# Optimization experiments

Measured on AMD Instinct MI355X. Metric: run time of the kernel, lower is better.

## Reference

```python
import jax, jax.numpy as jnp
import numpy as np

N = 100000      # nodes
E = 1600000     # edges
IN = 4          # input_size
H = 128         # hidden_channels
R = 20          # num_robots
OUT = 2         # output_size


def setup_inputs() -> dict:
    key = jax.random.key(0)
    ks = jax.random.split(key, 9)
    x = jax.random.normal(ks[0], (N, IN), dtype=jnp.float32)
    edge_index = jax.random.randint(ks[1], (2, E), 0, N, dtype=jnp.int32)
    batch = jnp.zeros((N,), dtype=jnp.int32)  # single graph
    # GCNConv weights (glorot-ish) and biases
    W1 = jax.random.normal(ks[2], (IN, H), dtype=jnp.float32) / np.sqrt(IN)
    b1 = jnp.zeros((H,), dtype=jnp.float32)
    W2 = jax.random.normal(ks[3], (H, H), dtype=jnp.float32) / np.sqrt(H)
    b2 = jnp.zeros((H,), dtype=jnp.float32)
    Wfc = jax.random.normal(ks[4], (H, OUT * R), dtype=jnp.float32) / np.sqrt(H)
    bfc = jnp.zeros((OUT * R,), dtype=jnp.float32)
    return {"x": x, "edge_index": edge_index, "batch": batch,
            "W1": W1, "b1": b1, "W2": W2, "b2": b2, "Wfc": Wfc, "bfc": bfc}


def gcn_conv(x, W, b, src, dst, n):
    # PyG GCNConv: h = x @ W, symmetric deg^-1/2 norm (self-loops already in src/dst),
    # aggregate messages at dst, then add bias.
    h = x @ W                                                     # [n, H_out]
    deg = jax.ops.segment_sum(jnp.ones(src.shape[0], h.dtype), dst, num_segments=n)
    dinv = jnp.where(deg > 0, jax.lax.rsqrt(deg), 0.0)            # [n]
    norm = dinv[src] * dinv[dst]                                  # [E+n]
    out = jax.ops.segment_sum(h[src] * norm[:, None], dst, num_segments=n)
    return out + b


def reference(x, edge_index, batch, W1, b1, W2, b2, Wfc, bfc):
    n = x.shape[0]
    loops = jnp.arange(n, dtype=edge_index.dtype)
    src = jnp.concatenate([edge_index[0], loops])   # add self-loops (GCNConv default)
    dst = jnp.concatenate([edge_index[1], loops])

    h = jnp.tanh(gcn_conv(x, W1, b1, src, dst, n))
    h = jnp.tanh(gcn_conv(h, W2, b2, src, dst, n))

    # global_mean_pool over batch (single graph)
    num_graphs = 1
    sums = jax.ops.segment_sum(h, batch, num_segments=num_graphs)           # [G, H]
    cnt = jax.ops.segment_sum(jnp.ones((n,), h.dtype), batch, num_segments=num_graphs)
    pooled = sums / jnp.maximum(cnt, 1.0)[:, None]

    vel = (pooled @ Wfc + bfc).reshape(-1, R, OUT)                          # [G, R, 2]

    # in_size = number of nodes with both first two features nonzero
    in_size = jnp.sum((x[:, 0] != 0.0) & (x[:, 1] != 0.0))
    mask = (jnp.arange(R) < in_size)[None, :, None]
    return jnp.where(mask, vel, 0.0)
```

## Files before the change

### kernel.cpp

```cpp
#include <hip/hip_runtime.h>
#include <hip/hip_fp16.h>

#define NN 100000
#define NE 1600000
#define INF 4
#define H 128
#define RR 20
#define OUTF 2
#define NB 782
#define NBP 784
#define EPB 4096
#define NBLK ((NE + EPB - 1) / EPB)
#define ASPLIT 4

typedef unsigned int uint32;
typedef __attribute__((ext_vector_type(8))) short short8;
typedef __attribute__((ext_vector_type(4))) float f32x4;

__device__ inline uint32 pack_f16(float x, float y) {
    return (uint32)__half_as_ushort(__float2half(x)) |
           ((uint32)__half_as_ushort(__float2half(y)) << 16);
}
__device__ inline __half2 bc_h2(uint32 u) {
    union { uint32 u; __half2 h; } c; c.u = u; return c.h;
}

__global__ void k_init_nodes(const float* __restrict__ x, int* __restrict__ in_size) {
    int i = blockIdx.x * 256 + threadIdx.x;
    bool pred = false;
    if (i < NN) {
        float x0 = x[(size_t)i * INF + 0];
        float x1 = x[(size_t)i * INF + 1];
        pred = (x0 != 0.f) && (x1 != 0.f);
    }
    unsigned long long m = __ballot(pred);
    if ((threadIdx.x & 63) == 0) {
        int c = __popcll(m);
        if (c) atomicAdd(in_size, c);
    }
}

__global__ void __launch_bounds__(256) k_hist(const int* __restrict__ dst,
                                              int* __restrict__ histG) {
    __shared__ int h[NB];
    int b = blockIdx.x, t = threadIdx.x;
    for (int i = t; i < NB; i += 256) h[i] = 0;
    __syncthreads();
    int e0 = b * EPB, eend = min(e0 + EPB, NE);
    for (int e = e0 + t; e < eend; e += 256) atomicAdd(&h[dst[e] >> 7], 1);
    __syncthreads();
    for (int i = t; i < NB; i += 256) histG[b * NBP + i] = h[i];
}

__global__ void k_btotoffs(const int* __restrict__ histG, int* __restrict__ offs,
                           int* __restrict__ btot) {
    int bkt = blockIdx.x * 256 + threadIdx.x;
    if (bkt >= NB) return;
    int run = 0;
    for (int j = 0; j < NBLK; ++j) {
        int v = histG[j * NBP + bkt];
        offs[j * NBP + bkt] = run;
        run += v;
    }
    btot[bkt] = run;
}

__global__ void __launch_bounds__(1024) k_bbase(const int* __restrict__ btot,
                                                int* __restrict__ bbase) {
    __shared__ int sm[1024];
    int t = threadIdx.x;
    int v = (t < NB) ? btot[t] : 0;
    sm[t] = v;
    __syncthreads();
    for (int off = 1; off < 1024; off <<= 1) {
        int u = (t >= off) ? sm[t - off] : 0;
        __syncthreads();
        sm[t] += u;
        __syncthreads();
    }
    if (t < NB) bbase[t] = sm[t] - v;
    if (t == 0) bbase[NB] = NE;
}

__global__ void __launch_bounds__(256) k_scat2(const int* __restrict__ src,
                                               const int* __restrict__ dst,
                                               const int* __restrict__ offs,
                                               const int* __restrict__ bbase,
                                               uint32* __restrict__ data) {
    __shared__ int cur[NB];
    int b = blockIdx.x, t = threadIdx.x;
    for (int i = t; i < NB; i += 256) cur[i] = offs[b * NBP + i] + bbase[i];
    __syncthreads();
    int e0 = b * EPB, eend = min(e0 + EPB, NE);
    for (int e = e0 + t; e < eend; e += 256) {
        int s = src[e], d = dst[e];
        int p = atomicAdd(&cur[d >> 7], 1);
        data[p] = ((uint32)s << 7) | (uint32)(d & 127);
    }
}

__global__ void __launch_bounds__(256) k_build(const uint32* __restrict__ data,
                                               const int* __restrict__ bbase,
                                               const float* __restrict__ x,
                                               int* __restrict__ csr_off,
                                               int* __restrict__ csr_cnt,
                                               int* __restrict__ csr_src,
                                               float* __restrict__ dinv,
                                               float4* __restrict__ xd) {
    __shared__ int hist[128], pfx[128], curs[128];
    int bkt = blockIdx.x;
    int t = threadIdx.x;
    int rbeg = bbase[bkt], rend = bbase[bkt + 1];
    if (t < 128) hist[t] = 0;
    __syncthreads();
    for (int j = rbeg + t; j < rend; j += 256)
        atomicAdd(&hist[data[j] & 127], 1);
    __syncthreads();
    if (t < 128) pfx[t] = hist[t];
    __syncthreads();
    for (int off = 1; off < 128; off <<= 1) {
        int u = (t < 128 && t >= off) ? pfx[t - off] : 0;
        __syncthreads();
        if (t < 128) pfx[t] += u;
        __syncthreads();
    }
    int nodeCount = min(128, NN - bkt * 128);
    if (t < nodeCount) {
        int gi = bkt * 128 + t;
        int excl = rbeg + pfx[t] - hist[t];
        csr_off[gi] = excl;
        csr_cnt[gi] = hist[t];
        curs[t] = excl;
        float di = rsqrtf((float)(hist[t] + 1));
        dinv[gi] = di;
        const float4 xv = *(const float4*)(x + (size_t)gi * INF);
        xd[gi] = make_float4(xv.x * di, xv.y * di, xv.z * di, xv.w * di);
    }
    __syncthreads();
    for (int j = rbeg + t; j < rend; j += 256) {
        uint32 r = data[j];
        int p = atomicAdd(&curs[r & 127], 1);
        csr_src[p] = (int)(r >> 7);
    }
}

__global__ void __launch_bounds__(256) k_aggx4(const uint32* __restrict__ data,
                                               const int* __restrict__ bbase,
                                               const float4* __restrict__ xd,
                                               float* __restrict__ Axpart) {
    __shared__ float acc[128][4];
    int bkt = blockIdx.x >> 2, sp = blockIdx.x & 3;
    int t = threadIdx.x;
    if (t < 128) { acc[t][0] = 0.f; acc[t][1] = 0.f; acc[t][2] = 0.f; acc[t][3] = 0.f; }
    int rbeg = bbase[bkt], rend = bbase[bkt + 1];
    int len = rend - rbeg;
    int q0 = rbeg + ((long long)len * sp >> 2);
    int q1 = rbeg + ((long long)len * (sp + 1) >> 2);
    __syncthreads();
    for (int j = q0 + t; j < q1; j += 256) {
        uint32 r = data[j];
        int s = (int)(r >> 7), dl = (int)(r & 127);
        const float4 v = xd[s];
        atomicAdd(&acc[dl][0], v.x);
        atomicAdd(&acc[dl][1], v.y);
        atomicAdd(&acc[dl][2], v.z);
        atomicAdd(&acc[dl][3], v.w);
    }
    __syncthreads();
    float* dstp = Axpart + (size_t)blockIdx.x * 512;
    for (int i = t; i < 512; i += 256) dstp[i] = ((const float*)acc)[i];
}

__global__ void k_merge(const float* __restrict__ Axpart, const float4* __restrict__ xd,
                        const float* __restrict__ dinv, float4* __restrict__ Ax) {
    int i = blockIdx.x * 256 + threadIdx.x;
    if (i >= NN) return;
    int bkt = i >> 7, nl = i & 127;
    float4 a = xd[i];
    #pragma unroll
    for (int sp = 0; sp < 4; ++sp) {
        const float4 p = *(const float4*)(Axpart + ((size_t)(bkt * 4 + sp)) * 512 + nl * 4);
        a.x += p.x; a.y += p.y; a.z += p.z; a.w += p.w;
    }
    float di = dinv[i];
    Ax[i] = make_float4(a.x * di, a.y * di, a.z * di, a.w * di);
}

__global__ void __launch_bounds__(256) k_mm1b(const float4* __restrict__ Ax,
                                              const float* __restrict__ dinv,
                                              const float* __restrict__ W1,
                                              const float* __restrict__ b1,
                                              uint32* __restrict__ Yp) {
    __shared__ float w1s[4][128];
    __shared__ float b1s[128];
    int t = threadIdx.x;
    if (t < 128) b1s[t] = b1[t];
    ((float*)w1s)[t] = W1[t];
    ((float*)w1s)[256 + t] = W1[256 + t];
    __syncthreads();
    int wid = t >> 6, lane = t & 63;
    int node = blockIdx.x * 4 + wid;
    if (node >= NN) return;
    const float4 a = Ax[node];
    float di = dinv[node];
    int f0 = lane * 2;
    float d0 = b1s[f0]     + a.x * w1s[0][f0]     + a.y * w1s[1][f0]
                           + a.z * w1s[2][f0]     + a.w * w1s[3][f0];
    float d1 = b1s[f0 + 1] + a.x * w1s[0][f0 + 1] + a.y * w1s[1][f0 + 1]
                           + a.z * w1s[2][f0 + 1] + a.w * w1s[3][f0 + 1];
    Yp[(size_t)node * 64 + lane] = pack_f16(tanhf(d0) * di, tanhf(d1) * di);
}

__global__ void k_aggy(const uint32* __restrict__ Yp, const int* __restrict__ csr_off,
                       const int* __restrict__ csr_cnt, const int* __restrict__ csr_src,
                       const float* __restrict__ dinv, uint32* __restrict__ Zp) {
    int wid = threadIdx.x >> 6;
    int lane = threadIdx.x & 63;
    int i = blockIdx.x * 4 + wid;
    if (i >= NN) return;
    int b = csr_off[i];
    int n = csr_cnt[i];
    int eg = lane >> 4, seg = lane & 15;

    __half2 h0 = bc_h2(0u), h1 = bc_h2(0u), h2 = bc_h2(0u), h3 = bc_h2(0u);
    int j = 0;
    for (; j + 16 <= n; j += 16) {
        int s0 = csr_src[b + j + eg];
        int s1 = csr_src[b + j + 4 + eg];
        int s2 = csr_src[b + j + 8 + eg];
        int s3 = csr_src[b + j + 12 + eg];
        uint4 v0 = *(const uint4*)(Yp + (size_t)s0 * 64 + seg * 4);
        uint4 v1 = *(const uint4*)(Yp + (size_t)s1 * 64 + seg * 4);
        uint4 v2 = *(const uint4*)(Yp + (size_t)s2 * 64 + seg * 4);
        uint4 v3 = *(const uint4*)(Yp + (size_t)s3 * 64 + seg * 4);
        h0 = __hadd2(h0, bc_h2(v0.x)); h1 = __hadd2(h1, bc_h2(v0.y));
        h2 = __hadd2(h2, bc_h2(v0.z)); h3 = __hadd2(h3, bc_h2(v0.w));
        h0 = __hadd2(h0, bc_h2(v1.x)); h1 = __hadd2(h1, bc_h2(v1.y));
        h2 = __hadd2(h2, bc_h2(v1.z)); h3 = __hadd2(h3, bc_h2(v1.w));
        h0 = __hadd2(h0, bc_h2(v2.x)); h1 = __hadd2(h1, bc_h2(v2.y));
        h2 = __hadd2(h2, bc_h2(v2.z)); h3 = __hadd2(h3, bc_h2(v2.w));
        h0 = __hadd2(h0, bc_h2(v3.x)); h1 = __hadd2(h1, bc_h2(v3.y));
        h2 = __hadd2(h2, bc_h2(v3.z)); h3 = __hadd2(h3, bc_h2(v3.w));
    }
    for (; j + 8 <= n; j += 8) {
        int s0 = csr_src[b + j + eg];
        int s1 = csr_src[b + j + 4 + eg];
        uint4 v0 = *(const uint4*)(Yp + (size_t)s0 * 64 + seg * 4);
        uint4 v1 = *(const uint4*)(Yp + (size_t)s1 * 64 + seg * 4);
        h0 = __hadd2(h0, bc_h2(v0.x)); h1 = __hadd2(h1, bc_h2(v0.y));
        h2 = __hadd2(h2, bc_h2(v0.z)); h3 = __hadd2(h3, bc_h2(v0.w));
        h0 = __hadd2(h0, bc_h2(v1.x)); h1 = __hadd2(h1, bc_h2(v1.y));
        h2 = __hadd2(h2, bc_h2(v1.z)); h3 = __hadd2(h3, bc_h2(v1.w));
    }
    for (; j < n; j += 4) {
        int jj = j + eg;
        bool valid = jj < n;
        int s = valid ? csr_src[b + jj] : i;
        uint4 v = *(const uint4*)(Yp + (size_t)s * 64 + seg * 4);
        if (valid) {
            h0 = __hadd2(h0, bc_h2(v.x)); h1 = __hadd2(h1, bc_h2(v.y));
            h2 = __hadd2(h2, bc_h2(v.z)); h3 = __hadd2(h3, bc_h2(v.w));
        }
    }
    {
        uint4 v = *(const uint4*)(Yp + (size_t)i * 64 + seg * 4);
        if (eg == 0) {
            h0 = __hadd2(h0, bc_h2(v.x)); h1 = __hadd2(h1, bc_h2(v.y));
            h2 = __hadd2(h2, bc_h2(v.z)); h3 = __hadd2(h3, bc_h2(v.w));
        }
    }
    float a[8];
    { float2 f = __half22float2(h0); a[0] = f.x; a[1] = f.y; }
    { float2 f = __half22float2(h1); a[2] = f.x; a[3] = f.y; }
    { float2 f = __half22float2(h2); a[4] = f.x; a[5] = f.y; }
    { float2 f = __half22float2(h3); a[6] = f.x; a[7] = f.y; }
    #pragma unroll
    for (int m = 0; m < 8; ++m) {
        a[m] += __shfl_xor(a[m], 16, 64);
        a[m] += __shfl_xor(a[m], 32, 64);
    }
    if (eg == 0) {
        float di = dinv[i];
        uint4 o;
        o.x = pack_f16(a[0] * di, a[1] * di);
        o.y = pack_f16(a[2] * di, a[3] * di);
        o.z = pack_f16(a[4] * di, a[5] * di);
        o.w = pack_f16(a[6] * di, a[7] * di);
        *(uint4*)(Zp + (size_t)i * 64 + seg * 4) = o;
    }
}

__global__ void __launch_bounds__(256) k_mm2pool(
    const uint32* __restrict__ Zp, const float* __restrict__ W2,
    const float* __restrict__ b2, float* __restrict__ pooled) {
    int tid = threadIdx.x;
    int wid = tid >> 6, lane = tid & 63;
    int nsub = lane & 15;
    int kg = lane >> 4;
    int fbase = wid * 32;

    short8 Bh[2][4], Bl[2][4];
    #pragma unroll
    for (int c = 0; c < 2; ++c) {
        #pragma unroll
        for (int ks = 0; ks < 4; ++ks) {
            short8 h, l;
            #pragma unroll
            for (int i = 0; i < 8; ++i) {
                float w = W2[(size_t)(ks * 32 + kg * 8 + i) * H + (fbase + c * 16 + nsub)];
                __half hh = __float2half(w);
                float wl = w - __half2float(hh);
                __half hl = __float2half(wl);
                h[i] = (short)__half_as_ushort(hh);
                l[i] = (short)__half_as_ushort(hl);
            }
            Bh[c][ks] = h;
            Bl[c][ks] = l;
        }
    }
    float bb0 = b2[fbase + nsub];
    float bb1 = b2[fbase + 16 + nsub];
    float pool0 = 0.f, pool1 = 0.f;

    const int ntiles = NN / 16;
    const int stride = (int)gridDim.x;
    int t = (int)blockIdx.x;

    short8 A[4];
    if (t < ntiles) {
        const uint32* rp = Zp + (size_t)(t * 16 + nsub) * 64 + kg * 4;
        #pragma unroll
        for (int ks = 0; ks < 4; ++ks) A[ks] = *(const short8*)(rp + ks * 16);
    }
    while (t < ntiles) {
        int tn = t + stride;
        short8 An[4];
        if (tn < ntiles) {
            const uint32* rp = Zp + (size_t)(tn * 16 + nsub) * 64 + kg * 4;
            #pragma unroll
            for (int ks = 0; ks < 4; ++ks) An[ks] = *(const short8*)(rp + ks * 16);
        }
        {
            f32x4 acch0 = {0.f,0.f,0.f,0.f}, accl0 = {0.f,0.f,0.f,0.f};
            f32x4 acch1 = {0.f,0.f,0.f,0.f}, accl1 = {0.f,0.f,0.f,0.f};
            #pragma unroll
            for (int ks = 0; ks < 4; ++ks) {
                acch0 = __builtin_amdgcn_mfma_f32_16x16x32_f16(A[ks], Bh[0][ks], acch0, 0, 0, 0);
                accl0 = __builtin_amdgcn_mfma_f32_16x16x32_f16(A[ks], Bl[0][ks], accl0, 0, 0, 0);
                acch1 = __builtin_amdgcn_mfma_f32_16x16x32_f16(A[ks], Bh[1][ks], acch1, 0, 0, 0);
                accl1 = __builtin_amdgcn_mfma_f32_16x16x32_f16(A[ks], Bl[1][ks], accl1, 0, 0, 0);
            }
            #pragma unroll
            for (int r = 0; r < 4; ++r) {
                pool0 += tanhf(acch0[r] + accl0[r] + bb0);
                pool1 += tanhf(acch1[r] + accl1[r] + bb1);
            }
        }
        #pragma unroll
        for (int ks = 0; ks < 4; ++ks) A[ks] = An[ks];
        t = tn;
    }

    pool0 += __shfl_xor(pool0, 16, 64);
    pool0 += __shfl_xor(pool0, 32, 64);
    pool1 += __shfl_xor(pool1, 16, 64);
    pool1 += __shfl_xor(pool1, 32, 64);
    if (kg == 0) {
        atomicAdd(&pooled[fbase + nsub], pool0);
        atomicAdd(&pooled[fbase + 16 + nsub], pool1);
    }
}

__global__ void k_final(const float* __restrict__ pooled, const float* __restrict__ Wfc,
                        const float* __restrict__ bfc, const int* __restrict__ in_size,
                        float* __restrict__ out) {
    int t = threadIdx.x;
    if (t >= RR * OUTF) return;
    const float invn = 1.0f / (float)NN;
    float a = bfc[t];
    for (int k = 0; k < H; ++k) a += (pooled[k] * invn) * Wfc[k * (RR * OUTF) + t];
    int r = t >> 1;
    out[t] = (r < *in_size) ? a : 0.f;
}

extern "C" void kernel_launch(void* const* d_in, const int* in_sizes, int n_in,
                              void* d_out, int out_size, void* d_ws, size_t ws_size,
                              hipStream_t stream) {
    const float* x   = (const float*)d_in[0];
    const int*   ei  = (const int*)d_in[1];
    const float* W1  = (const float*)d_in[3];
    const float* b1  = (const float*)d_in[4];
    const float* W2  = (const float*)d_in[5];
    const float* b2  = (const float*)d_in[6];
    const float* Wfc = (const float*)d_in[7];
    const float* bfc = (const float*)d_in[8];
    float* out = (float*)d_out;

    const int* srcp = ei;
    const int* dstp = ei + NE;

    char* ws = (char*)d_ws;
    size_t off = 0;
    auto alloc = [&](size_t bytes) { void* p = ws + off; off += (bytes + 511) & ~(size_t)511; return p; };
    float*  pooled  = (float*)alloc(H * 4);
    int*    in_size = (int*)alloc(64);
    int*    histG   = (int*)alloc((size_t)NBLK * NBP * 4);
    int*    offs    = (int*)alloc((size_t)NBLK * NBP * 4);
    int*    btot    = (int*)alloc((size_t)NB * 4);
    int*    bbase   = (int*)alloc(((size_t)NB + 1) * 4);
    uint32* data    = (uint32*)alloc((size_t)NE * 4);
    float*  dinv    = (float*)alloc((size_t)NN * 4);
    float4* xd      = (float4*)alloc((size_t)NN * 16);
    int*    csr_off = (int*)alloc((size_t)NN * 4);
    int*    csr_cnt = (int*)alloc((size_t)NN * 4);
    int*    csr_src = (int*)alloc((size_t)NE * 4);
    float*  Axpart  = (float*)alloc((size_t)NB * ASPLIT * 512 * 4);
    float4* Ax      = (float4*)alloc((size_t)NN * 16);
    uint32* Yp      = (uint32*)alloc((size_t)NN * 64 * 4);
    uint32* Zp      = (uint32*)alloc((size_t)NN * 64 * 4);
    (void)off; (void)ws_size; (void)in_sizes; (void)n_in; (void)out_size;

    const int nbN = (NN + 255) / 256;
    const int nbW = (NN + 3) / 4;

    hipMemsetAsync(pooled, 0, 1024, stream);
    k_init_nodes<<<nbN, 256, 0, stream>>>(x, in_size);
    k_hist<<<NBLK, 256, 0, stream>>>(dstp, histG);
    k_btotoffs<<<(NB + 255) / 256, 256, 0, stream>>>(histG, offs, btot);
    k_bbase<<<1, 1024, 0, stream>>>(btot, bbase);
    k_scat2<<<NBLK, 256, 0, stream>>>(srcp, dstp, offs, bbase, data);
    k_build<<<NB, 256, 0, stream>>>(data, bbase, x, csr_off, csr_cnt, csr_src, dinv, xd);
    k_aggx4<<<NB * ASPLIT, 256, 0, stream>>>(data, bbase, xd, Axpart);
    k_merge<<<nbN, 256, 0, stream>>>(Axpart, xd, dinv, Ax);
    k_mm1b<<<nbW, 256, 0, stream>>>(Ax, dinv, W1, b1, Yp);
    k_aggy<<<nbW, 256, 0, stream>>>(Yp, csr_off, csr_cnt, csr_src, dinv, Zp);
    k_mm2pool<<<512, 256, 0, stream>>>(Zp, W2, b2, pooled);
    k_final<<<1, 64, 0, stream>>>(pooled, Wfc, bfc, in_size, out);
}
```

Before: 323.2 us.

## Fuse preprocessing kernels and merge partial sums into the first matmul

Folds the in_size count into k_build, combines the two scan kernels into a single-block k_scan, and fuses the Axpart merge into a per-bucket layer-1 matmul kernel that stages aggregated features in shared memory. This removes three kernel launches and the Ax intermediate round-trip through global memory. It also raises edges per block from 4096 to 16384, which shrinks the histogram and offset arrays and the serial scan length. The cost is far fewer blocks in k_hist and k_scat2, so those two stages have less parallelism.

```diff
diff --git a/kernel.cpp b/kernel.cpp
--- a/kernel.cpp
+++ b/kernel.cpp
@@ -9,7 +9,7 @@
 #define OUTF 2
 #define NB 782
 #define NBP 784
-#define EPB 4096
+#define EPB 16384
 #define NBLK ((NE + EPB - 1) / EPB)
 #define ASPLIT 4
 
@@ -23,21 +23,6 @@
 }
 __device__ inline __half2 bc_h2(uint32 u) {
     union { uint32 u; __half2 h; } c; c.u = u; return c.h;
-}
-
-__global__ void k_init_nodes(const float* __restrict__ x, int* __restrict__ in_size) {
-    int i = blockIdx.x * 256 + threadIdx.x;
-    bool pred = false;
-    if (i < NN) {
-        float x0 = x[(size_t)i * INF + 0];
-        float x1 = x[(size_t)i * INF + 1];
-        pred = (x0 != 0.f) && (x1 != 0.f);
-    }
-    unsigned long long m = __ballot(pred);
-    if ((threadIdx.x & 63) == 0) {
-        int c = __popcll(m);
-        if (c) atomicAdd(in_size, c);
-    }
 }
 
 __global__ void __launch_bounds__(256) k_hist(const int* __restrict__ dst,
@@ -52,25 +37,20 @@
     for (int i = t; i < NB; i += 256) histG[b * NBP + i] = h[i];
 }
 
-__global__ void k_btotoffs(const int* __restrict__ histG, int* __restrict__ offs,
-                           int* __restrict__ btot) {
-    int bkt = blockIdx.x * 256 + threadIdx.x;
-    if (bkt >= NB) return;
-    int run = 0;
-    for (int j = 0; j < NBLK; ++j) {
-        int v = histG[j * NBP + bkt];
-        offs[j * NBP + bkt] = run;
-        run += v;
-    }
-    btot[bkt] = run;
-}
-
-__global__ void __launch_bounds__(1024) k_bbase(const int* __restrict__ btot,
-                                                int* __restrict__ bbase) {
+__global__ void __launch_bounds__(1024) k_scan(const int* __restrict__ histG,
+                                               int* __restrict__ offs,
+                                               int* __restrict__ bbase) {
     __shared__ int sm[1024];
     int t = threadIdx.x;
-    int v = (t < NB) ? btot[t] : 0;
-    sm[t] = v;
+    int run = 0;
+    if (t < NB) {
+        for (int j = 0; j < NBLK; ++j) {
+            int v = histG[j * NBP + t];
+            offs[j * NBP + t] = run;
+            run += v;
+        }
+    }
+    sm[t] = (t < NB) ? run : 0;
     __syncthreads();
     for (int off = 1; off < 1024; off <<= 1) {
         int u = (t >= off) ? sm[t - off] : 0;
@@ -78,7 +58,7 @@
         sm[t] += u;
         __syncthreads();
     }
-    if (t < NB) bbase[t] = sm[t] - v;
+    if (t < NB) bbase[t] = sm[t] - run;
     if (t == 0) bbase[NB] = NE;
 }
 
@@ -106,7 +86,8 @@
                                                int* __restrict__ csr_cnt,
                                                int* __restrict__ csr_src,
                                                float* __restrict__ dinv,
-                                               float4* __restrict__ xd) {
+                                               float4* __restrict__ xd,
+                                               int* __restrict__ in_size) {
     __shared__ int hist[128], pfx[128], curs[128];
     int bkt = blockIdx.x;
     int t = threadIdx.x;
@@ -125,6 +106,7 @@
         __syncthreads();
     }
     int nodeCount = min(128, NN - bkt * 128);
+    bool pred = false;
     if (t < nodeCount) {
         int gi = bkt * 128 + t;
         int excl = rbeg + pfx[t] - hist[t];
@@ -135,6 +117,12 @@
         dinv[gi] = di;
         const float4 xv = *(const float4*)(x + (size_t)gi * INF);
         xd[gi] = make_float4(xv.x * di, xv.y * di, xv.z * di, xv.w * di);
+        pred = (xv.x != 0.f) && (xv.y != 0.f);
+    }
+    unsigned long long m = __ballot(pred);
+    if ((t & 63) == 0) {
+        int c = __popcll(m);
+        if (c) atomicAdd(in_size, c);
     }
     __syncthreads();
     for (int j = rbeg + t; j < rend; j += 256) {
@@ -171,44 +159,55 @@
     for (int i = t; i < 512; i += 256) dstp[i] = ((const float*)acc)[i];
 }
 
-__global__ void k_merge(const float* __restrict__ Axpart, const float4* __restrict__ xd,
-                        const float* __restrict__ dinv, float4* __restrict__ Ax) {
-    int i = blockIdx.x * 256 + threadIdx.x;
-    if (i >= NN) return;
-    int bkt = i >> 7, nl = i & 127;
-    float4 a = xd[i];
-    #pragma unroll
-    for (int sp = 0; sp < 4; ++sp) {
-        const float4 p = *(const float4*)(Axpart + ((size_t)(bkt * 4 + sp)) * 512 + nl * 4);
-        a.x += p.x; a.y += p.y; a.z += p.z; a.w += p.w;
-    }
-    float di = dinv[i];
-    Ax[i] = make_float4(a.x * di, a.y * di, a.z * di, a.w * di);
-}
-
-__global__ void __launch_bounds__(256) k_mm1b(const float4* __restrict__ Ax,
+__global__ void __launch_bounds__(256) k_mm1c(const float* __restrict__ Axpart,
+                                              const float4* __restrict__ xd,
                                               const float* __restrict__ dinv,
                                               const float* __restrict__ W1,
                                               const float* __restrict__ b1,
                                               uint32* __restrict__ Yp) {
+    __shared__ float axs[128][4];
+    __shared__ float ds[128];
     __shared__ float w1s[4][128];
     __shared__ float b1s[128];
+    int bkt = blockIdx.x;
     int t = threadIdx.x;
     if (t < 128) b1s[t] = b1[t];
     ((float*)w1s)[t] = W1[t];
     ((float*)w1s)[256 + t] = W1[256 + t];
-    __syncthreads();
-    int wid = t >> 6, lane = t & 63;
-    int node = blockIdx.x * 4 + wid;
-    if (node >= NN) return;
-    const float4 a = Ax[node];
-    float di = dinv[node];
-    int f0 = lane * 2;
-    float d0 = b1s[f0]     + a.x * w1s[0][f0]     + a.y * w1s[1][f0]
-                           + a.z * w1s[2][f0]     + a.w * w1s[3][f0];
-    float d1 = b1s[f0 + 1] + a.x * w1s[0][f0 + 1] + a.y * w1s[1][f0 + 1]
-                           + a.z * w1s[2][f0 + 1] + a.w * w1s[3][f0 + 1];
-    Yp[(size_t)node * 64 + lane] = pack_f16(tanhf(d0) * di, tanhf(d1) * di);
+    int nodeCount = min(128, NN - bkt * 128);
+    if (t < nodeCount) {
+        int gi = bkt * 128 + t;
+        float4 a = xd[gi];
+        #pragma unroll
+        for (int sp = 0; sp < 4; ++sp) {
+            const float4 p = *(const float4*)(Axpart + ((size_t)(bkt * 4 + sp)) * 512 + t * 4);
+            a.x += p.x; a.y += p.y; a.z += p.z; a.w += p.w;
+        }
+        float di = dinv[gi];
+        axs[t][0] = a.x * di; axs[t][1] = a.y * di;
+        axs[t][2] = a.z * di; axs[t][3] = a.w * di;
+        ds[t] = di;
+    }
+    __syncthreads();
+    int nbase = bkt * 128;
+    #pragma unroll
+    for (int rep = 0; rep < 32; ++rep) {
+        int flat = rep * 256 + t;
+        int node = flat >> 6;
+        int fp = flat & 63;
+        int gi = nbase + node;
+        if (gi < NN) {
+            float a0 = axs[node][0], a1 = axs[node][1];
+            float a2 = axs[node][2], a3 = axs[node][3];
+            float di = ds[node];
+            int f0 = fp * 2;
+            float d0 = b1s[f0]     + a0 * w1s[0][f0]     + a1 * w1s[1][f0]
+                                   + a2 * w1s[2][f0]     + a3 * w1s[3][f0];
+            float d1 = b1s[f0 + 1] + a0 * w1s[0][f0 + 1] + a1 * w1s[1][f0 + 1]
+                                   + a2 * w1s[2][f0 + 1] + a3 * w1s[3][f0 + 1];
+            Yp[(size_t)gi * 64 + fp] = pack_f16(tanhf(d0) * di, tanhf(d1) * di);
+        }
+    }
 }
 
 __global__ void k_aggy(const uint32* __restrict__ Yp, const int* __restrict__ csr_off,
@@ -406,7 +405,6 @@
     int*    in_size = (int*)alloc(64);
     int*    histG   = (int*)alloc((size_t)NBLK * NBP * 4);
     int*    offs    = (int*)alloc((size_t)NBLK * NBP * 4);
-    int*    btot    = (int*)alloc((size_t)NB * 4);
     int*    bbase   = (int*)alloc(((size_t)NB + 1) * 4);
     uint32* data    = (uint32*)alloc((size_t)NE * 4);
     float*  dinv    = (float*)alloc((size_t)NN * 4);
@@ -415,24 +413,19 @@
     int*    csr_cnt = (int*)alloc((size_t)NN * 4);
     int*    csr_src = (int*)alloc((size_t)NE * 4);
     float*  Axpart  = (float*)alloc((size_t)NB * ASPLIT * 512 * 4);
-    float4* Ax      = (float4*)alloc((size_t)NN * 16);
     uint32* Yp      = (uint32*)alloc((size_t)NN * 64 * 4);
     uint32* Zp      = (uint32*)alloc((size_t)NN * 64 * 4);
     (void)off; (void)ws_size; (void)in_sizes; (void)n_in; (void)out_size;
 
-    const int nbN = (NN + 255) / 256;
     const int nbW = (NN + 3) / 4;
 
     hipMemsetAsync(pooled, 0, 1024, stream);
-    k_init_nodes<<<nbN, 256, 0, stream>>>(x, in_size);
     k_hist<<<NBLK, 256, 0, stream>>>(dstp, histG);
-    k_btotoffs<<<(NB + 255) / 256, 256, 0, stream>>>(histG, offs, btot);
-    k_bbase<<<1, 1024, 0, stream>>>(btot, bbase);
+    k_scan<<<1, 1024, 0, stream>>>(histG, offs, bbase);
     k_scat2<<<NBLK, 256, 0, stream>>>(srcp, dstp, offs, bbase, data);
-    k_build<<<NB, 256, 0, stream>>>(data, bbase, x, csr_off, csr_cnt, csr_src, dinv, xd);
+    k_build<<<NB, 256, 0, stream>>>(data, bbase, x, csr_off, csr_cnt, csr_src, dinv, xd, in_size);
     k_aggx4<<<NB * ASPLIT, 256, 0, stream>>>(data, bbase, xd, Axpart);
-    k_merge<<<nbN, 256, 0, stream>>>(Axpart, xd, dinv, Ax);
-    k_mm1b<<<nbW, 256, 0, stream>>>(Ax, dinv, W1, b1, Yp);
+    k_mm1c<<<NB, 256, 0, stream>>>(Axpart, xd, dinv, W1, b1, Yp);
     k_aggy<<<nbW, 256, 0, stream>>>(Yp, csr_off, csr_cnt, csr_src, dinv, Zp);
     k_mm2pool<<<512, 256, 0, stream>>>(Zp, W2, b2, pooled);
     k_final<<<1, 64, 0, stream>>>(pooled, Wfc, bfc, in_size, out);
```

Result: faster. 309.9 us (-4.1%).
